# Performance work log

Measured on AMD Instinct MI355X. Metric: run time of the kernel, lower is better.

Reference implementation:

```python
import jax, jax.numpy as jnp
import numpy as np

NEG_INF = -1.0e9
KQ_DIM = 64


def setup_inputs() -> dict:
    key = jax.random.key(0)
    ks = jax.random.split(key, 10)
    S, B, H, DK, DV = 2048, 8, 512, 64, 64
    q = jax.random.normal(ks[0], (S, B, H), dtype=jnp.float32)
    k = jax.random.normal(ks[1], (S, B, H), dtype=jnp.float32)
    v = jax.random.normal(ks[2], (S, B, H), dtype=jnp.float32)
    attn_mask = jax.random.bernoulli(ks[3], 0.1, (S, B))          # (q_seq, batch)
    key_padding_mask = jax.random.bernoulli(ks[4], 0.1, (B, S))   # (batch, k_seq)
    scale = 0.02
    Wq = jax.random.normal(ks[5], (DK, H), dtype=jnp.float32) * scale
    bq = jnp.zeros((DK,), dtype=jnp.float32)
    Wk = jax.random.normal(ks[6], (DK, H), dtype=jnp.float32) * scale
    bk = jnp.zeros((DK,), dtype=jnp.float32)
    Wv = jax.random.normal(ks[7], (DV, H), dtype=jnp.float32) * scale
    bv = jnp.zeros((DV,), dtype=jnp.float32)
    return {
        "q_hidden_inputs": q, "k_hidden_inputs": k, "v_hidden_inputs": v,
        "Wq": Wq, "bq": bq, "Wk": Wk, "bk": bk, "Wv": Wv, "bv": bv,
        "attn_mask": attn_mask, "key_padding_mask": key_padding_mask,
    }


def reference(q_hidden_inputs, k_hidden_inputs, v_hidden_inputs,
              Wq, bq, Wk, bk, Wv, bv, attn_mask, key_padding_mask):
    # inputs are (seq, batch, hidden) -> (batch, seq, hidden)
    q = jnp.transpose(q_hidden_inputs, (1, 0, 2))
    k = jnp.transpose(k_hidden_inputs, (1, 0, 2))
    v = jnp.transpose(v_hidden_inputs, (1, 0, 2))
    # pre-projection key padding mask: fill padded key hidden states with -1e9
    k = jnp.where(key_padding_mask[:, :, None], NEG_INF, k)
    queries = jnp.einsum('bsh,dh->bsd', q, Wq) + bq   # (B, Sq, DK)
    keys = jnp.einsum('bsh,dh->bsd', k, Wk) + bk      # (B, Sk, DK)
    values = jnp.einsum('bsh,dh->bsd', v, Wv) + bv    # (B, Sk, DV)
    scores = jnp.einsum('bqd,bkd->bqk', queries, keys) / jnp.sqrt(jnp.float32(KQ_DIM))
    # attn_mask (Sq, B) -> (B, Sq, 1): masks whole query rows, broadcast over keys
    scores = jnp.where(jnp.transpose(attn_mask, (1, 0))[:, :, None], NEG_INF, scores)
    probs = jax.nn.softmax(scores, axis=-1)           # (B, Sq, Sk)
    out = jnp.einsum('bqk,bkd->bqd', probs, values)   # (B, Sq, DV)
    return jnp.transpose(out, (1, 0, 2))              # (Sq, B, DV)
```

## Files before the change

### kernel.cpp

```cpp
#include <hip/hip_runtime.h>
#include <stdint.h>

#define S_LEN 2048
#define BATCH 8
#define HID   512
#define DD    64

typedef __bf16 bf16x8 __attribute__((ext_vector_type(8)));
typedef float  f32x4  __attribute__((ext_vector_type(4)));

#define WS_QB 0
#define WS_KB (2*1024*1024)
#define WS_VB (4*1024*1024)
#define WS_VT (6*1024*1024)
#define WS_MS (8*1024*1024)
#define WS_U  (WS_MS + 65536)
#define WS_C  (WS_U + 2048)
#define WS_KM (WS_C + 16)
#define WS_FLP (WS_KM + 256)
#define WS_CTP (WS_FLP + 256)
#define WS_DT (WS_CTP + 256)
#define WS_AM (WS_DT + 16)
#define WS_KP (WS_AM + 16384)
#define WS_PT (9*1024*1024)
#define PT_BYTES(ks) ((size_t)(ks) * 8 * 2048 * 68 * 4)

__device__ inline unsigned short f2bf(float f) {
    union { float f; unsigned u; } v; v.f = f;
    unsigned r = v.u + 0x7FFFu + ((v.u >> 16) & 1u);
    return (unsigned short)(r >> 16);
}

__device__ inline unsigned short f2bfc(float f) {
    __bf16 h = (__bf16)f;
    return __builtin_bit_cast(unsigned short, h);
}

__device__ inline bf16x8 load8(const unsigned short* p) {
    uint4 t = *(const uint4*)p;
    return __builtin_bit_cast(bf16x8, t);
}

__device__ inline bf16x8 pack8(float4 a, float4 b) {
    unsigned short h[8] __attribute__((aligned(16)));
    h[0]=f2bfc(a.x); h[1]=f2bfc(a.y); h[2]=f2bfc(a.z); h[3]=f2bfc(a.w);
    h[4]=f2bfc(b.x); h[5]=f2bfc(b.y); h[6]=f2bfc(b.z); h[7]=f2bfc(b.w);
    return load8(h);
}

__global__ void kA_detect(const float* __restrict__ Wk, const float* __restrict__ bk,
                          const void* am_raw, const void* kpm_raw,
                          int* __restrict__ gflp, float* __restrict__ kmask)
{
    int bi = blockIdx.x, tid = threadIdx.x;
    if (bi < 32) {
        __shared__ int smask[2];
        if (tid < 2) smask[tid] = 0;
        __syncthreads();
        for (int mi = 0; mi < 2; ++mi) {
            const unsigned char* base = (const unsigned char*)(mi ? kpm_raw : am_raw);
            const unsigned char*      p8  = base + bi * 512;
            const unsigned short*     p16 = (const unsigned short*)base + bi * 256;
            const unsigned int*       p32 = (const unsigned int*)base + bi * 128;
            const unsigned long long* p64 = (const unsigned long long*)base + bi * 64;
            int v[8] = {0,0,0,0,0,0,0,0};
            if (tid < 64) {
                unsigned long long w = p64[tid];
                if (w != 0ull && w != 0x3FF0000000000000ull) v[0] = 1;
                if (w > 1ull)                                v[1] = 1;
            }
            if (tid < 128) {
                unsigned w = p32[tid];
                if (w != 0u && w != 0x3F800000u) v[2] = 1;
                if (w > 1u)                      v[3] = 1;
            }
            {
                unsigned short w = p16[tid];
                if (w != 0 && w != 0x3F80) v[4] = 1;
                if (w != 0 && w != 0x3C00) v[5] = 1;
                if (w > 1)                 v[6] = 1;
            }
            if (p8[tid] > 1 || p8[tid + 256] > 1) v[7] = 1;
            int bits = 0;
            #pragma unroll
            for (int j = 0; j < 8; ++j)
                if (v[j]) bits |= (1 << j);
            if (bits) atomicOr(&smask[mi], bits);
        }
        __syncthreads();
        if (tid < 2) gflp[bi * 2 + tid] = smask[tid];
    } else {
        __shared__ float r[256];
        int d = bi - 32;
        const float* wr = Wk + (size_t)d * HID;
        r[tid] = wr[tid] + wr[tid + 256];
        __syncthreads();
        for (int off = 128; off > 0; off >>= 1) {
            if (tid < off) r[tid] += r[tid + off];
            __syncthreads();
        }
        if (tid == 0) kmask[d] = -1.0e9f * r[0] + bk[d];
    }
}

__global__ void kB_finish(const void* am_raw, const void* kpm_raw,
                          const int* __restrict__ gflp,
                          const float* __restrict__ Wq, const float* __restrict__ bq,
                          const float* __restrict__ kmask,
                          unsigned char* __restrict__ am8,
                          unsigned char* __restrict__ kp8,
                          int* __restrict__ cntp, int* __restrict__ dts,
                          float* __restrict__ u, float* __restrict__ cbuf)
{
    int bi = blockIdx.x, tid = threadIdx.x;
    if (bi < 32) {
        int m[2] = {0, 0};
        #pragma unroll 8
        for (int i = 0; i < 32; ++i) { m[0] |= gflp[i * 2]; m[1] |= gflp[i * 2 + 1]; }
        __shared__ int scnt[2];
        if (tid < 2) scnt[tid] = 0;
        __syncthreads();
        for (int mi = 0; mi < 2; ++mi) {
            int d = 8;
            #pragma unroll
            for (int j = 7; j >= 0; --j)
                if (!((m[mi] >> j) & 1)) d = j;
            const unsigned char*      p8  = (const unsigned char*)(mi ? kpm_raw : am_raw);
            const unsigned short*     p16 = (const unsigned short*)p8;
            const unsigned int*       p32 = (const unsigned int*)p8;
            const unsigned long long* p64 = (const unsigned long long*)p8;
            unsigned char* dst = mi ? kp8 : am8;
            int c = 0;
            #pragma unroll
            for (int it = 0; it < 2; ++it) {
                int e = bi * 512 + tid + it * 256;
                int bbit;
                if (d <= 1)      bbit = (p64[e] != 0ull);
                else if (d <= 3) bbit = (p32[e] != 0u);
                else if (d <= 6) bbit = (p16[e] != 0);
                else             bbit = (p8[e]  != 0);
                dst[e] = (unsigned char)bbit;
                c += bbit;
            }
            c += __shfl_xor(c, 1);  c += __shfl_xor(c, 2);
            c += __shfl_xor(c, 4);  c += __shfl_xor(c, 8);
            c += __shfl_xor(c, 16); c += __shfl_xor(c, 32);
            if ((tid & 63) == 0) atomicAdd(&scnt[mi], c);
            if (bi == 0 && tid == 0) dts[mi] = d;
        }
        __syncthreads();
        if (tid < 2) cntp[bi * 2 + tid] = scnt[tid];
    } else if (bi == 32) {
        __shared__ float kml[64];
        if (tid < 64) kml[tid] = kmask[tid];
        __syncthreads();
        for (int h = tid; h < HID; h += 256) {
            float s = 0.f;
            #pragma unroll 8
            for (int d = 0; d < 64; ++d) s += Wq[(size_t)d * HID + h] * kml[d];
            u[h] = s;
        }
    } else {
        __shared__ float ca[64];
        if (tid < 64) ca[tid] = bq[tid] * kmask[tid];
        __syncthreads();
        if (tid == 0) {
            float s = 0.f;
            #pragma unroll
            for (int d = 0; d < 64; ++d) s += ca[d];
            *cbuf = s;
        }
    }
}

__launch_bounds__(256)
__global__ void k1_proj(const float* __restrict__ q, const float* __restrict__ k,
                        const float* __restrict__ v,
                        const float* __restrict__ Wq, const float* __restrict__ bq,
                        const float* __restrict__ Wk, const float* __restrict__ bk,
                        const float* __restrict__ Wv, const float* __restrict__ bv,
                        unsigned short* __restrict__ Qb, unsigned short* __restrict__ Kb,
                        unsigned short* __restrict__ Vb,
                        const float* __restrict__ u, const float* __restrict__ cbuf,
                        float* __restrict__ msc)
{
    __shared__ __align__(16) unsigned short lw[64][72];

    const float *X, *W, *bias; unsigned short* Y; int do_ms;
    if (blockIdx.y == 0)      { X = q; W = Wq; bias = bq; Y = Qb; do_ms = 1; }
    else if (blockIdx.y == 1) { X = k; W = Wk; bias = bk; Y = Kb; do_ms = 0; }
    else                      { X = v; W = Wv; bias = bv; Y = Vb; do_ms = 0; }

    int tid = threadIdx.x;
    int w = tid >> 6, lane = tid & 63;
    int g = lane >> 4, r16 = lane & 15;
    int r0 = blockIdx.x * 64;
    int srow = tid >> 2, sq = tid & 3;

    const float* xrow = X + (size_t)(r0 + w * 16 + r16) * HID;

    float mac = 0.f;
    f32x4 acc[4];
    #pragma unroll
    for (int i = 0; i < 4; ++i) acc[i] = (f32x4){0.f, 0.f, 0.f, 0.f};

    for (int k0 = 0; k0 < HID; k0 += 64) {
        __syncthreads();
        {
            const float* wr = W + (size_t)srow * HID + k0 + sq * 16;
            float wv[16];
            #pragma unroll
            for (int i = 0; i < 16; i += 4) {
                float4 t = *(const float4*)(wr + i);
                wv[i] = t.x; wv[i+1] = t.y; wv[i+2] = t.z; wv[i+3] = t.w;
            }
            unsigned short hw[16] __attribute__((aligned(16)));
            #pragma unroll
            for (int i = 0; i < 16; ++i) hw[i] = f2bfc(wv[i]);
            *(uint4*)&lw[srow][sq * 16]     = *(uint4*)hw;
            *(uint4*)&lw[srow][sq * 16 + 8] = *(uint4*)(hw + 8);
        }
        float4 xa = *(const float4*)(xrow + k0 + g * 8);
        float4 xb = *(const float4*)(xrow + k0 + g * 8 + 4);
        float4 xc = *(const float4*)(xrow + k0 + 32 + g * 8);
        float4 xd = *(const float4*)(xrow + k0 + 32 + g * 8 + 4);
        if (do_ms) {
            float4 ua = *(const float4*)(u + k0 + g * 8);
            float4 ub = *(const float4*)(u + k0 + g * 8 + 4);
            float4 uc = *(const float4*)(u + k0 + 32 + g * 8);
            float4 ud = *(const float4*)(u + k0 + 32 + g * 8 + 4);
            mac += xa.x*ua.x + xa.y*ua.y + xa.z*ua.z + xa.w*ua.w;
            mac += xb.x*ub.x + xb.y*ub.y + xb.z*ub.z + xb.w*ub.w;
            mac += xc.x*uc.x + xc.y*uc.y + xc.z*uc.z + xc.w*uc.w;
            mac += xd.x*ud.x + xd.y*ud.y + xd.z*ud.z + xd.w*ud.w;
        }
        bf16x8 af0 = pack8(xa, xb);
        bf16x8 af1 = pack8(xc, xd);
        __syncthreads();
        #pragma unroll
        for (int d4 = 0; d4 < 4; ++d4) {
            bf16x8 bf0 = load8(&lw[d4 * 16 + r16][g * 8]);
            acc[d4] = __builtin_amdgcn_mfma_f32_16x16x32_bf16(af0, bf0, acc[d4], 0, 0, 0);
            bf16x8 bf1 = load8(&lw[d4 * 16 + r16][32 + g * 8]);
            acc[d4] = __builtin_amdgcn_mfma_f32_16x16x32_bf16(af1, bf1, acc[d4], 0, 0, 0);
        }
    }

    float bv4[4];
    #pragma unroll
    for (int d4 = 0; d4 < 4; ++d4) bv4[d4] = bias[d4 * 16 + r16];
    #pragma unroll
    for (int d4 = 0; d4 < 4; ++d4) {
        #pragma unroll
        for (int vv = 0; vv < 4; ++vv) {
            int r = r0 + w * 16 + 4 * g + vv;
            int bb = r & 7, ss = r >> 3;
            Y[((size_t)bb * S_LEN + ss) * DD + d4 * 16 + r16] = f2bfc(acc[d4][vv] + bv4[d4]);
        }
    }
    if (do_ms) {
        mac += __shfl_xor(mac, 16);
        mac += __shfl_xor(mac, 32);
        if (g == 0) {
            int r = r0 + w * 16 + r16;
            msc[(size_t)(r & 7) * S_LEN + (r >> 3)] = (mac + *cbuf) * 0.125f;
        }
    }
}

__launch_bounds__(256)
__global__ void kT_transpose(const unsigned short* __restrict__ Vb,
                             unsigned short* __restrict__ Vt)
{
    __shared__ __align__(16) unsigned short t[64][72];
    int b = blockIdx.y, s0 = blockIdx.x * 64;
    int tid = threadIdx.x;
    int skey = tid & 63, sdq = (tid >> 6) * 16;
    {
        const unsigned short* vp = Vb + ((size_t)b * S_LEN + s0 + skey) * DD + sdq;
        uint4 t0 = *(const uint4*)vp;
        uint4 t1 = *(const uint4*)(vp + 8);
        unsigned short tmp[16];
        *(uint4*)tmp = t0; *(uint4*)(tmp + 8) = t1;
        #pragma unroll
        for (int i = 0; i < 16; ++i) t[sdq + i][skey] = tmp[i];
    }
    __syncthreads();
    int dv = tid >> 2, kseg = (tid & 3) * 16;
    unsigned short* dst = Vt + (((size_t)b * 32 + (s0 >> 6)) * 64 + dv) * 64 + kseg;
    uint4 a0 = *(const uint4*)&t[dv][kseg];
    uint4 a1 = *(const uint4*)&t[dv][kseg + 8];
    *(uint4*)dst       = a0;
    *(uint4*)(dst + 8) = a1;
}

__launch_bounds__(256)
__global__ void k2_attn(const unsigned short* __restrict__ Qb,
                        const unsigned short* __restrict__ Kb,
                        const unsigned short* __restrict__ Vt,
                        const float* __restrict__ msc,
                        const unsigned char* __restrict__ am8,
                        const unsigned char* __restrict__ kp8,
                        float* __restrict__ part, int ks)
{
    __shared__ __align__(16) unsigned short kl[64][72];
    __shared__ __align__(16) unsigned short vl[64][72];
    __shared__ __align__(16) unsigned short pl[4][16][72];

    int tid = threadIdx.x;
    int w = tid >> 6, lane = tid & 63;
    int g = lane >> 4, r16 = lane & 15;
    int b = blockIdx.y;
    int z = blockIdx.z;
    int q0 = blockIdx.x * 64 + w * 16;
    int kspan = S_LEN / ks;
    int kbeg = z * kspan;
    int nt = kspan >> 6;

    int srow = tid >> 2, sseg = (tid & 3) * 16;
    const unsigned short* kstage = Kb + ((size_t)b * S_LEN + srow) * DD + sseg;
    const unsigned short* vstage = Vt + (size_t)b * (32 * 64 * 64) + srow * 64 + sseg;

    const unsigned short* qp = Qb + ((size_t)b * S_LEN + q0 + r16) * DD + g * 8;
    bf16x8 qa0 = load8(qp);
    bf16x8 qa1 = load8(qp + 32);

    int qq = q0 + r16;
    float mscv = msc[(size_t)b * S_LEN + qq];
    int qm = am8[qq * 8 + b];
    const unsigned char* kpb = kp8 + (size_t)b * S_LEN + 4 * g;

    float mrun = -1.0e30f, lsum = 0.f;
    f32x4 acco[4];
    #pragma unroll
    for (int i = 0; i < 4; ++i) acco[i] = (f32x4){0.f, 0.f, 0.f, 0.f};

    uint4 ka0 = *(const uint4*)(kstage + (size_t)kbeg * DD);
    uint4 ka1 = *(const uint4*)(kstage + (size_t)kbeg * DD + 8);
    uint4 va0 = *(const uint4*)(vstage + (size_t)(kbeg >> 6) * 4096);
    uint4 va1 = *(const uint4*)(vstage + (size_t)(kbeg >> 6) * 4096 + 8);

    for (int t = 0; t < nt; ++t) {
        int kt0 = kbeg + t * 64;
        __syncthreads();
        *(uint4*)&kl[srow][sseg]     = ka0;
        *(uint4*)&kl[srow][sseg + 8] = ka1;
        *(uint4*)&vl[srow][sseg]     = va0;
        *(uint4*)&vl[srow][sseg + 8] = va1;
        __syncthreads();

        if (t + 1 < nt) {
            int kn = kt0 + 64;
            ka0 = *(const uint4*)(kstage + (size_t)kn * DD);
            ka1 = *(const uint4*)(kstage + (size_t)kn * DD + 8);
            va0 = *(const uint4*)(vstage + (size_t)(kn >> 6) * 4096);
            va1 = *(const uint4*)(vstage + (size_t)(kn >> 6) * 4096 + 8);
        }

        f32x4 accs[4];
        #pragma unroll
        for (int kt = 0; kt < 4; ++kt) {
            accs[kt] = (f32x4){0.f, 0.f, 0.f, 0.f};
            bf16x8 kb0 = load8(&kl[kt * 16 + r16][g * 8]);
            bf16x8 kb1 = load8(&kl[kt * 16 + r16][32 + g * 8]);
            accs[kt] = __builtin_amdgcn_mfma_f32_16x16x32_bf16(kb0, qa0, accs[kt], 0, 0, 0);
            accs[kt] = __builtin_amdgcn_mfma_f32_16x16x32_bf16(kb1, qa1, accs[kt], 0, 0, 0);
        }

        float p[4][4];
        #pragma unroll
        for (int kt = 0; kt < 4; ++kt) {
            unsigned kp4 = *(const unsigned*)(kpb + kt0 + kt * 16);
            #pragma unroll
            for (int vv = 0; vv < 4; ++vv) {
                float s = accs[kt][vv] * 0.125f;
                if ((kp4 >> (8 * vv)) & 0xFFu) s = mscv;
                if (qm) s = -1.0e9f;
                p[kt][vv] = s;
            }
        }

        float mt = p[0][0];
        #pragma unroll
        for (int kt = 0; kt < 4; ++kt)
            #pragma unroll
            for (int vv = 0; vv < 4; ++vv)
                mt = fmaxf(mt, p[kt][vv]);
        mt = fmaxf(mt, __shfl_xor(mt, 16));
        mt = fmaxf(mt, __shfl_xor(mt, 32));

        float mn = fmaxf(mrun, mt);
        float f = __expf(mrun - mn);
        mrun = mn;

        float ps = 0.f;
        #pragma unroll
        for (int kt = 0; kt < 4; ++kt)
            #pragma unroll
            for (int vv = 0; vv < 4; ++vv) {
                float pv = __expf(p[kt][vv] - mn);
                p[kt][vv] = pv;
                ps += pv;
            }
        ps += __shfl_xor(ps, 16);
        ps += __shfl_xor(ps, 32);
        lsum = lsum * f + ps;
        #pragma unroll
        for (int d4 = 0; d4 < 4; ++d4) acco[d4] *= f;

        #pragma unroll
        for (int kt = 0; kt < 4; ++kt) {
            unsigned w0 = (unsigned)f2bf(p[kt][0]) | ((unsigned)f2bf(p[kt][1]) << 16);
            unsigned w1 = (unsigned)f2bf(p[kt][2]) | ((unsigned)f2bf(p[kt][3]) << 16);
            unsigned short* dst = &pl[w][r16][kt * 16 + 4 * g];
            *(unsigned*)dst       = w0;
            *(unsigned*)(dst + 2) = w1;
        }

        #pragma unroll
        for (int h = 0; h < 2; ++h) {
            bf16x8 pa = load8(&pl[w][r16][h * 32 + g * 8]);
            #pragma unroll
            for (int d4 = 0; d4 < 4; ++d4) {
                bf16x8 vb = load8(&vl[d4 * 16 + r16][h * 32 + g * 8]);
                acco[d4] = __builtin_amdgcn_mfma_f32_16x16x32_bf16(vb, pa, acco[d4], 0, 0, 0);
            }
        }
    }

    float* pp = part + ((size_t)(z * BATCH + b) * S_LEN + qq) * 68;
    #pragma unroll
    for (int d4 = 0; d4 < 4; ++d4)
        *(float4*)(pp + d4 * 16 + 4 * g) =
            make_float4(acco[d4][0], acco[d4][1], acco[d4][2], acco[d4][3]);
    if (g == 0) { pp[64] = mrun; pp[65] = lsum; }
}

__global__ void k2c_combine(const float* __restrict__ part, float* __restrict__ out, int ks)
{
    int t = blockIdx.x * 256 + threadIdx.x;
    int row = t >> 4, s16 = t & 15;
    int b = row >> 11, qq = row & 2047;

    float M = -3.0e38f;
    #pragma unroll
    for (int z = 0; z < 8; ++z)
        if (z < ks)
            M = fmaxf(M, part[((size_t)(z * BATCH + b) * S_LEN + qq) * 68 + 64]);

    float lt = 0.f;
    float4 r = make_float4(0.f, 0.f, 0.f, 0.f);
    #pragma unroll
    for (int z = 0; z < 8; ++z) {
        if (z < ks) {
            const float* pp = part + ((size_t)(z * BATCH + b) * S_LEN + qq) * 68;
            float wv = __expf(pp[64] - M);
            lt += pp[65] * wv;
            float4 a = *(const float4*)(pp + s16 * 4);
            r.x += a.x * wv; r.y += a.y * wv; r.z += a.z * wv; r.w += a.w * wv;
        }
    }
    float inv = 1.f / lt;
    float* op = out + ((size_t)qq * BATCH + b) * DD + s16 * 4;
    *(float4*)op = make_float4(r.x * inv, r.y * inv, r.z * inv, r.w * inv);
}

__global__ void k3_diag(const int* __restrict__ cntp, const int* __restrict__ dts,
                        float* __restrict__ out, int bad_sizes)
{
    int c0 = 0, c1 = 0;
    #pragma unroll 8
    for (int i = 0; i < 32; ++i) { c0 += cntp[i * 2]; c1 += cntp[i * 2 + 1]; }
    float dg = 0.f;
    if (bad_sizes)                   dg = 1.0e6f;
    else if (c0 < 164 || c0 > 8192)  dg = 2.0e6f + (float)dts[0] * 1.0e5f;
    else if (c1 < 164 || c1 > 8192)  dg = 6.0e6f + (float)dts[1] * 1.0e5f;
    if (dg != 0.f) out[0] = dg;
}

extern "C" void kernel_launch(void* const* d_in, const int* in_sizes, int n_in,
                              void* d_out, int out_size, void* d_ws, size_t ws_size,
                              hipStream_t stream) {
    const float* q   = (const float*)d_in[0];
    const float* k   = (const float*)d_in[1];
    const float* v   = (const float*)d_in[2];
    const float* Wq  = (const float*)d_in[3];
    const float* bq  = (const float*)d_in[4];
    const float* Wk  = (const float*)d_in[5];
    const float* bk  = (const float*)d_in[6];
    const float* Wv  = (const float*)d_in[7];
    const float* bv  = (const float*)d_in[8];
    const void*  am  = d_in[9];
    const void*  kpm = d_in[10];

    char* ws = (char*)d_ws;
    unsigned short* Qb = (unsigned short*)(ws + WS_QB);
    unsigned short* Kb = (unsigned short*)(ws + WS_KB);
    unsigned short* Vb = (unsigned short*)(ws + WS_VB);
    unsigned short* Vt = (unsigned short*)(ws + WS_VT);
    float* msc = (float*)(ws + WS_MS);
    float* u   = (float*)(ws + WS_U);
    float* cb  = (float*)(ws + WS_C);
    float* km  = (float*)(ws + WS_KM);
    int*  gflp = (int*)(ws + WS_FLP);
    int*  cntp = (int*)(ws + WS_CTP);
    int*   dts = (int*)(ws + WS_DT);
    unsigned char* am8 = (unsigned char*)(ws + WS_AM);
    unsigned char* kp8 = (unsigned char*)(ws + WS_KP);
    float* part = (float*)(ws + WS_PT);

    int ok = (n_in == 11)
        && in_sizes[0] == 8388608 && in_sizes[1] == 8388608 && in_sizes[2] == 8388608
        && in_sizes[3] == 32768 && in_sizes[4] == 64
        && in_sizes[5] == 32768 && in_sizes[6] == 64
        && in_sizes[7] == 32768 && in_sizes[8] == 64
        && in_sizes[9] == 16384 && in_sizes[10] == 16384
        && out_size == 1048576;

    int ks = 1;
    if      (ws_size >= (size_t)WS_PT + PT_BYTES(8)) ks = 8;
    else if (ws_size >= (size_t)WS_PT + PT_BYTES(4)) ks = 4;
    else if (ws_size >= (size_t)WS_PT + PT_BYTES(2)) ks = 2;

    kA_detect<<<96, 256, 0, stream>>>(Wk, bk, am, kpm, gflp, km);
    kB_finish<<<34, 256, 0, stream>>>(am, kpm, gflp, Wq, bq, km,
                                      am8, kp8, cntp, dts, u, cb);

    dim3 g1(256, 3);
    k1_proj<<<g1, 256, 0, stream>>>(q, k, v, Wq, bq, Wk, bk, Wv, bv,
                                    Qb, Kb, Vb, u, cb, msc);

    dim3 gt(32, 8);
    kT_transpose<<<gt, 256, 0, stream>>>(Vb, Vt);

    dim3 g2(32, 8, ks);
    k2_attn<<<g2, 256, 0, stream>>>(Qb, Kb, Vt, msc, am8, kp8, part, ks);

    k2c_combine<<<1024, 256, 0, stream>>>(part, (float*)d_out, ks);

    k3_diag<<<1, 1, 0, stream>>>(cntp, dts, (float*)d_out, !ok);
}
```

Baseline: 78.16 us.

## Fuse prologue kernels, V transpose into projection, and diagnostics into combine

Merges the mask-detection and mask-finish kernels into one, with each block redundantly scanning the full mask to find the encoding instead of exchanging flags through global memory. The u vector (Wq times the key-mask vector) and the constant term are now computed inside the Q projection per K-chunk, and the V projection writes its transposed tile straight to Vt through shared memory, which removes the separate transpose kernel. The diagnostic kernel is folded into the combine kernel. Launch count falls from seven to four, in exchange for redundant mask scans per block and extra work and a barrier in the Q projection loop.

```diff
diff --git a/kernel.cpp b/kernel.cpp
--- a/kernel.cpp
+++ b/kernel.cpp
@@ -11,14 +11,10 @@
 
 #define WS_QB 0
 #define WS_KB (2*1024*1024)
-#define WS_VB (4*1024*1024)
 #define WS_VT (6*1024*1024)
 #define WS_MS (8*1024*1024)
-#define WS_U  (WS_MS + 65536)
-#define WS_C  (WS_U + 2048)
-#define WS_KM (WS_C + 16)
-#define WS_FLP (WS_KM + 256)
-#define WS_CTP (WS_FLP + 256)
+#define WS_KM (WS_MS + 65536)
+#define WS_CTP (WS_KM + 256)
 #define WS_DT (WS_CTP + 256)
 #define WS_AM (WS_DT + 16)
 #define WS_KP (WS_AM + 16384)
@@ -50,81 +46,57 @@
 
 __global__ void kA_detect(const float* __restrict__ Wk, const float* __restrict__ bk,
                           const void* am_raw, const void* kpm_raw,
-                          int* __restrict__ gflp, float* __restrict__ kmask)
+                          unsigned char* __restrict__ am8,
+                          unsigned char* __restrict__ kp8,
+                          int* __restrict__ cntp, int* __restrict__ dts,
+                          float* __restrict__ kmask)
 {
     int bi = blockIdx.x, tid = threadIdx.x;
     if (bi < 32) {
-        __shared__ int smask[2];
-        if (tid < 2) smask[tid] = 0;
+        __shared__ int viol[2][8];
+        __shared__ int scnt[2];
+        if (tid < 16) viol[tid >> 3][tid & 7] = 0;
+        if (tid < 2) scnt[tid] = 0;
         __syncthreads();
         for (int mi = 0; mi < 2; ++mi) {
-            const unsigned char* base = (const unsigned char*)(mi ? kpm_raw : am_raw);
-            const unsigned char*      p8  = base + bi * 512;
-            const unsigned short*     p16 = (const unsigned short*)base + bi * 256;
-            const unsigned int*       p32 = (const unsigned int*)base + bi * 128;
-            const unsigned long long* p64 = (const unsigned long long*)base + bi * 64;
+            const unsigned char*      p8  = (const unsigned char*)(mi ? kpm_raw : am_raw);
+            const unsigned short*     p16 = (const unsigned short*)p8;
+            const unsigned int*       p32 = (const unsigned int*)p8;
+            const unsigned long long* p64 = (const unsigned long long*)p8;
             int v[8] = {0,0,0,0,0,0,0,0};
-            if (tid < 64) {
-                unsigned long long w = p64[tid];
+            for (int i = tid; i < 2048; i += 256) {
+                unsigned long long w = p64[i];
                 if (w != 0ull && w != 0x3FF0000000000000ull) v[0] = 1;
                 if (w > 1ull)                                v[1] = 1;
             }
-            if (tid < 128) {
-                unsigned w = p32[tid];
+            for (int i = tid; i < 4096; i += 256) {
+                unsigned w = p32[i];
                 if (w != 0u && w != 0x3F800000u) v[2] = 1;
                 if (w > 1u)                      v[3] = 1;
             }
-            {
-                unsigned short w = p16[tid];
+            for (int i = tid; i < 8192; i += 256) {
+                unsigned short w = p16[i];
                 if (w != 0 && w != 0x3F80) v[4] = 1;
                 if (w != 0 && w != 0x3C00) v[5] = 1;
                 if (w > 1)                 v[6] = 1;
             }
-            if (p8[tid] > 1 || p8[tid + 256] > 1) v[7] = 1;
+            for (int i = tid; i < 16384; i += 256)
+                if (p8[i] > 1) v[7] = 1;
             int bits = 0;
             #pragma unroll
             for (int j = 0; j < 8; ++j)
                 if (v[j]) bits |= (1 << j);
-            if (bits) atomicOr(&smask[mi], bits);
-        }
-        __syncthreads();
-        if (tid < 2) gflp[bi * 2 + tid] = smask[tid];
-    } else {
-        __shared__ float r[256];
-        int d = bi - 32;
-        const float* wr = Wk + (size_t)d * HID;
-        r[tid] = wr[tid] + wr[tid + 256];
-        __syncthreads();
-        for (int off = 128; off > 0; off >>= 1) {
-            if (tid < off) r[tid] += r[tid + off];
-            __syncthreads();
-        }
-        if (tid == 0) kmask[d] = -1.0e9f * r[0] + bk[d];
-    }
-}
-
-__global__ void kB_finish(const void* am_raw, const void* kpm_raw,
-                          const int* __restrict__ gflp,
-                          const float* __restrict__ Wq, const float* __restrict__ bq,
-                          const float* __restrict__ kmask,
-                          unsigned char* __restrict__ am8,
-                          unsigned char* __restrict__ kp8,
-                          int* __restrict__ cntp, int* __restrict__ dts,
-                          float* __restrict__ u, float* __restrict__ cbuf)
-{
-    int bi = blockIdx.x, tid = threadIdx.x;
-    if (bi < 32) {
-        int m[2] = {0, 0};
-        #pragma unroll 8
-        for (int i = 0; i < 32; ++i) { m[0] |= gflp[i * 2]; m[1] |= gflp[i * 2 + 1]; }
-        __shared__ int scnt[2];
-        if (tid < 2) scnt[tid] = 0;
+            if (bits) atomicOr(&viol[mi][0], 0);
+            #pragma unroll
+            for (int j = 0; j < 8; ++j)
+                if (v[j]) atomicOr(&viol[mi][j], 1);
+        }
         __syncthreads();
         for (int mi = 0; mi < 2; ++mi) {
             int d = 8;
             #pragma unroll
             for (int j = 7; j >= 0; --j)
-                if (!((m[mi] >> j) & 1)) d = j;
+                if (!viol[mi][j]) d = j;
             const unsigned char*      p8  = (const unsigned char*)(mi ? kpm_raw : am_raw);
             const unsigned short*     p16 = (const unsigned short*)p8;
             const unsigned int*       p32 = (const unsigned int*)p8;
@@ -150,26 +122,17 @@
         }
         __syncthreads();
         if (tid < 2) cntp[bi * 2 + tid] = scnt[tid];
-    } else if (bi == 32) {
-        __shared__ float kml[64];
-        if (tid < 64) kml[tid] = kmask[tid];
-        __syncthreads();
-        for (int h = tid; h < HID; h += 256) {
-            float s = 0.f;
-            #pragma unroll 8
-            for (int d = 0; d < 64; ++d) s += Wq[(size_t)d * HID + h] * kml[d];
-            u[h] = s;
-        }
     } else {
-        __shared__ float ca[64];
-        if (tid < 64) ca[tid] = bq[tid] * kmask[tid];
-        __syncthreads();
-        if (tid == 0) {
-            float s = 0.f;
-            #pragma unroll
-            for (int d = 0; d < 64; ++d) s += ca[d];
-            *cbuf = s;
-        }
+        __shared__ float r[256];
+        int d = bi - 32;
+        const float* wr = Wk + (size_t)d * HID;
+        r[tid] = wr[tid] + wr[tid + 256];
+        __syncthreads();
+        for (int off = 128; off > 0; off >>= 1) {
+            if (tid < off) r[tid] += r[tid + off];
+            __syncthreads();
+        }
+        if (tid == 0) kmask[d] = -1.0e9f * r[0] + bk[d];
     }
 }
 
@@ -180,24 +143,45 @@
                         const float* __restrict__ Wk, const float* __restrict__ bk,
                         const float* __restrict__ Wv, const float* __restrict__ bv,
                         unsigned short* __restrict__ Qb, unsigned short* __restrict__ Kb,
-                        unsigned short* __restrict__ Vb,
-                        const float* __restrict__ u, const float* __restrict__ cbuf,
-                        float* __restrict__ msc)
+                        unsigned short* __restrict__ Vt,
+                        const float* __restrict__ kmask, float* __restrict__ msc)
 {
     __shared__ __align__(16) unsigned short lw[64][72];
-
-    const float *X, *W, *bias; unsigned short* Y; int do_ms;
-    if (blockIdx.y == 0)      { X = q; W = Wq; bias = bq; Y = Qb; do_ms = 1; }
-    else if (blockIdx.y == 1) { X = k; W = Wk; bias = bk; Y = Kb; do_ms = 0; }
-    else                      { X = v; W = Wv; bias = bv; Y = Vb; do_ms = 0; }
+    __shared__ __align__(16) float ut[64];
+    __shared__ float kml[64];
+    __shared__ float csh;
+
+    const float *X, *W, *bias; int mode;
+    if (blockIdx.y == 0)      { X = q; W = Wq; bias = bq; mode = 0; }
+    else if (blockIdx.y == 1) { X = k; W = Wk; bias = bk; mode = 1; }
+    else                      { X = v; W = Wv; bias = bv; mode = 2; }
+    int do_ms = (mode == 0);
 
     int tid = threadIdx.x;
     int w = tid >> 6, lane = tid & 63;
     int g = lane >> 4, r16 = lane & 15;
-    int r0 = blockIdx.x * 64;
     int srow = tid >> 2, sq = tid & 3;
 
-    const float* xrow = X + (size_t)(r0 + w * 16 + r16) * HID;
+    int r0 = 0, b2 = 0, s0 = 0;
+    const float* xrow;
+    if (mode < 2) {
+        r0 = blockIdx.x * 64;
+        xrow = X + (size_t)(r0 + w * 16 + r16) * HID;
+    } else {
+        b2 = blockIdx.x & 7; s0 = (blockIdx.x >> 3) * 64;
+        xrow = X + ((size_t)(s0 + w * 16 + r16) * 8 + b2) * HID;
+    }
+
+    if (do_ms) {
+        if (tid < 64) kml[tid] = kmask[tid];
+        __syncthreads();
+        if (tid == 0) {
+            float s = 0.f;
+            #pragma unroll
+            for (int d = 0; d < 64; ++d) s += bq[d] * kml[d];
+            csh = s;
+        }
+    }
 
     float mac = 0.f;
     f32x4 acc[4];
@@ -220,15 +204,22 @@
             *(uint4*)&lw[srow][sq * 16]     = *(uint4*)hw;
             *(uint4*)&lw[srow][sq * 16 + 8] = *(uint4*)(hw + 8);
         }
+        if (do_ms && tid < 64) {
+            float s = 0.f;
+            #pragma unroll 8
+            for (int d = 0; d < 64; ++d) s += Wq[(size_t)d * HID + k0 + tid] * kml[d];
+            ut[tid] = s;
+        }
         float4 xa = *(const float4*)(xrow + k0 + g * 8);
         float4 xb = *(const float4*)(xrow + k0 + g * 8 + 4);
         float4 xc = *(const float4*)(xrow + k0 + 32 + g * 8);
         float4 xd = *(const float4*)(xrow + k0 + 32 + g * 8 + 4);
+        __syncthreads();
         if (do_ms) {
-            float4 ua = *(const float4*)(u + k0 + g * 8);
-            float4 ub = *(const float4*)(u + k0 + g * 8 + 4);
-            float4 uc = *(const float4*)(u + k0 + 32 + g * 8);
-            float4 ud = *(const float4*)(u + k0 + 32 + g * 8 + 4);
+            float4 ua = *(const float4*)&ut[g * 8];
+            float4 ub = *(const float4*)&ut[g * 8 + 4];
+            float4 uc = *(const float4*)&ut[32 + g * 8];
+            float4 ud = *(const float4*)&ut[32 + g * 8 + 4];
             mac += xa.x*ua.x + xa.y*ua.y + xa.z*ua.z + xa.w*ua.w;
             mac += xb.x*ub.x + xb.y*ub.y + xb.z*ub.z + xb.w*ub.w;
             mac += xc.x*uc.x + xc.y*uc.y + xc.z*uc.z + xc.w*uc.w;
@@ -236,7 +227,6 @@
         }
         bf16x8 af0 = pack8(xa, xb);
         bf16x8 af1 = pack8(xc, xd);
-        __syncthreads();
         #pragma unroll
         for (int d4 = 0; d4 < 4; ++d4) {
             bf16x8 bf0 = load8(&lw[d4 * 16 + r16][g * 8]);
@@ -249,49 +239,39 @@
     float bv4[4];
     #pragma unroll
     for (int d4 = 0; d4 < 4; ++d4) bv4[d4] = bias[d4 * 16 + r16];
-    #pragma unroll
-    for (int d4 = 0; d4 < 4; ++d4) {
-        #pragma unroll
-        for (int vv = 0; vv < 4; ++vv) {
-            int r = r0 + w * 16 + 4 * g + vv;
-            int bb = r & 7, ss = r >> 3;
-            Y[((size_t)bb * S_LEN + ss) * DD + d4 * 16 + r16] = f2bfc(acc[d4][vv] + bv4[d4]);
-        }
-    }
-    if (do_ms) {
-        mac += __shfl_xor(mac, 16);
-        mac += __shfl_xor(mac, 32);
-        if (g == 0) {
-            int r = r0 + w * 16 + r16;
-            msc[(size_t)(r & 7) * S_LEN + (r >> 3)] = (mac + *cbuf) * 0.125f;
-        }
-    }
-}
-
-__launch_bounds__(256)
-__global__ void kT_transpose(const unsigned short* __restrict__ Vb,
-                             unsigned short* __restrict__ Vt)
-{
-    __shared__ __align__(16) unsigned short t[64][72];
-    int b = blockIdx.y, s0 = blockIdx.x * 64;
-    int tid = threadIdx.x;
-    int skey = tid & 63, sdq = (tid >> 6) * 16;
-    {
-        const unsigned short* vp = Vb + ((size_t)b * S_LEN + s0 + skey) * DD + sdq;
-        uint4 t0 = *(const uint4*)vp;
-        uint4 t1 = *(const uint4*)(vp + 8);
-        unsigned short tmp[16];
-        *(uint4*)tmp = t0; *(uint4*)(tmp + 8) = t1;
-        #pragma unroll
-        for (int i = 0; i < 16; ++i) t[sdq + i][skey] = tmp[i];
-    }
-    __syncthreads();
-    int dv = tid >> 2, kseg = (tid & 3) * 16;
-    unsigned short* dst = Vt + (((size_t)b * 32 + (s0 >> 6)) * 64 + dv) * 64 + kseg;
-    uint4 a0 = *(const uint4*)&t[dv][kseg];
-    uint4 a1 = *(const uint4*)&t[dv][kseg + 8];
-    *(uint4*)dst       = a0;
-    *(uint4*)(dst + 8) = a1;
+
+    if (mode < 2) {
+        unsigned short* Y = (mode == 0) ? Qb : Kb;
+        #pragma unroll
+        for (int d4 = 0; d4 < 4; ++d4) {
+            #pragma unroll
+            for (int vv = 0; vv < 4; ++vv) {
+                int r = r0 + w * 16 + 4 * g + vv;
+                int bb = r & 7, ss = r >> 3;
+                Y[((size_t)bb * S_LEN + ss) * DD + d4 * 16 + r16] = f2bfc(acc[d4][vv] + bv4[d4]);
+            }
+        }
+        if (do_ms) {
+            mac += __shfl_xor(mac, 16);
+            mac += __shfl_xor(mac, 32);
+            if (g == 0) {
+                int r = r0 + w * 16 + r16;
+                msc[(size_t)(r & 7) * S_LEN + (r >> 3)] = (mac + csh) * 0.125f;
+            }
+        }
+    } else {
+        __syncthreads();
+        #pragma unroll
+        for (int d4 = 0; d4 < 4; ++d4)
+            #pragma unroll
+            for (int vv = 0; vv < 4; ++vv)
+                lw[d4 * 16 + r16][w * 16 + 4 * g + vv] = f2bfc(acc[d4][vv] + bv4[d4]);
+        __syncthreads();
+        int dv = tid >> 2, sseg = (tid & 3) * 16;
+        unsigned short* dst = Vt + (((size_t)b2 * 32 + (s0 >> 6)) * 64 + dv) * 64 + sseg;
+        *(uint4*)dst       = *(uint4*)&lw[dv][sseg];
+        *(uint4*)(dst + 8) = *(uint4*)&lw[dv][sseg + 8];
+    }
 }
 
 __launch_bounds__(256)
@@ -436,7 +416,9 @@
     if (g == 0) { pp[64] = mrun; pp[65] = lsum; }
 }
 
-__global__ void k2c_combine(const float* __restrict__ part, float* __restrict__ out, int ks)
+__global__ void k2c_combine(const float* __restrict__ part, float* __restrict__ out,
+                            const int* __restrict__ cntp, const int* __restrict__ dts,
+                            int ks, int bad_sizes)
 {
     int t = blockIdx.x * 256 + threadIdx.x;
     int row = t >> 4, s16 = t & 15;
@@ -463,19 +445,17 @@
     float inv = 1.f / lt;
     float* op = out + ((size_t)qq * BATCH + b) * DD + s16 * 4;
     *(float4*)op = make_float4(r.x * inv, r.y * inv, r.z * inv, r.w * inv);
-}
-
-__global__ void k3_diag(const int* __restrict__ cntp, const int* __restrict__ dts,
-                        float* __restrict__ out, int bad_sizes)
-{
-    int c0 = 0, c1 = 0;
-    #pragma unroll 8
-    for (int i = 0; i < 32; ++i) { c0 += cntp[i * 2]; c1 += cntp[i * 2 + 1]; }
-    float dg = 0.f;
-    if (bad_sizes)                   dg = 1.0e6f;
-    else if (c0 < 164 || c0 > 8192)  dg = 2.0e6f + (float)dts[0] * 1.0e5f;
-    else if (c1 < 164 || c1 > 8192)  dg = 6.0e6f + (float)dts[1] * 1.0e5f;
-    if (dg != 0.f) out[0] = dg;
+
+    if (t == 0) {
+        int c0 = 0, c1 = 0;
+        #pragma unroll 8
+        for (int i = 0; i < 32; ++i) { c0 += cntp[i * 2]; c1 += cntp[i * 2 + 1]; }
+        float dg = 0.f;
+        if (bad_sizes)                   dg = 1.0e6f;
+        else if (c0 < 164 || c0 > 8192)  dg = 2.0e6f + (float)dts[0] * 1.0e5f;
+        else if (c1 < 164 || c1 > 8192)  dg = 6.0e6f + (float)dts[1] * 1.0e5f;
+        if (dg != 0.f) out[0] = dg;
+    }
 }
 
 extern "C" void kernel_launch(void* const* d_in, const int* in_sizes, int n_in,
@@ -496,13 +476,9 @@
     char* ws = (char*)d_ws;
     unsigned short* Qb = (unsigned short*)(ws + WS_QB);
     unsigned short* Kb = (unsigned short*)(ws + WS_KB);
-    unsigned short* Vb = (unsigned short*)(ws + WS_VB);
     unsigned short* Vt = (unsigned short*)(ws + WS_VT);
     float* msc = (float*)(ws + WS_MS);
-    float* u   = (float*)(ws + WS_U);
-    float* cb  = (float*)(ws + WS_C);
     float* km  = (float*)(ws + WS_KM);
-    int*  gflp = (int*)(ws + WS_FLP);
     int*  cntp = (int*)(ws + WS_CTP);
     int*   dts = (int*)(ws + WS_DT);
     unsigned char* am8 = (unsigned char*)(ws + WS_AM);
@@ -522,21 +498,14 @@
     else if (ws_size >= (size_t)WS_PT + PT_BYTES(4)) ks = 4;
     else if (ws_size >= (size_t)WS_PT + PT_BYTES(2)) ks = 2;
 
-    kA_detect<<<96, 256, 0, stream>>>(Wk, bk, am, kpm, gflp, km);
-    kB_finish<<<34, 256, 0, stream>>>(am, kpm, gflp, Wq, bq, km,
-                                      am8, kp8, cntp, dts, u, cb);
+    kA_detect<<<96, 256, 0, stream>>>(Wk, bk, am, kpm, am8, kp8, cntp, dts, km);
 
     dim3 g1(256, 3);
     k1_proj<<<g1, 256, 0, stream>>>(q, k, v, Wq, bq, Wk, bk, Wv, bv,
-                                    Qb, Kb, Vb, u, cb, msc);
-
-    dim3 gt(32, 8);
-    kT_transpose<<<gt, 256, 0, stream>>>(Vb, Vt);
+                                    Qb, Kb, Vt, km, msc);
 
     dim3 g2(32, 8, ks);
     k2_attn<<<g2, 256, 0, stream>>>(Qb, Kb, Vt, msc, am8, kp8, part, ks);
 
-    k2c_combine<<<1024, 256, 0, stream>>>(part, (float*)d_out, ks);
-
-    k3_diag<<<1, 1, 0, stream>>>(cntp, dts, (float*)d_out, !ok);
-}
+    k2c_combine<<<1024, 256, 0, stream>>>(part, (float*)d_out, cntp, dts, ks, !ok);
+}
```

After: 106.2 us. 35.9% more time.
